# Kernel tuning notes

Measured on AMD Instinct MI355X. Metric: run time of the kernel, lower is better.

The kernel has to match this reference:

```python
import jax, jax.numpy as jnp
import numpy as np

B, M, K, F, H = 4096, 50000, 31, 256, 256
N = K + 1                      # nodes per graph: center + K neighbors
GAMMA = 1.0 / (2.0 * 1.0 ** 2) # rbf_kernel gamma with length_scale = 1.0


def setup_inputs() -> dict:
    key = jax.random.key(0)
    k = jax.random.split(key, 9)
    return {
        "spatial_features": jax.random.normal(k[0], (B, 2), jnp.float32),
        "features": jax.random.normal(k[1], (B, F), jnp.float32),
        "train_spatial": jax.random.normal(k[2], (M, 2), jnp.float32),
        "train_features": jax.random.normal(k[3], (M, F), jnp.float32),
        "train_y": jax.random.normal(k[4], (M, 1), jnp.float32),
        "W0": jax.random.normal(k[5], (F + 2, H), jnp.float32) * (1.0 / np.sqrt(F + 2)),
        "W1": jax.random.normal(k[6], (H, H), jnp.float32) * (1.0 / np.sqrt(H)),
        "W2": jax.random.normal(k[7], (H, H), jnp.float32) * (1.0 / np.sqrt(H)),
        "Wout": jax.random.normal(k[8], (H, 1), jnp.float32) * (1.0 / np.sqrt(H)),
    }


def reference(spatial_features, features, train_spatial, train_features, train_y,
              W0, W1, W2, Wout):
    # --- brute-force kNN over train spatial coords (sklearn kneighbors) ---
    d2 = (jnp.sum(spatial_features ** 2, -1, keepdims=True)
          - 2.0 * spatial_features @ train_spatial.T
          + jnp.sum(train_spatial ** 2, -1)[None, :])                 # [B, M]
    nb = jax.lax.top_k(jax.lax.stop_gradient(-d2), K)[1]              # [B, K] indices

    # --- form_input_graph: node features = [feat ++ y ++ indicator] ---
    feat = jnp.concatenate([features[:, None, :], train_features[nb]], axis=1)    # [B,N,F]
    y = jnp.concatenate([jnp.zeros((B, 1, 1), feat.dtype), train_y[nb]], axis=1)  # [B,N,1]
    ind = jnp.zeros((B, N, 1), feat.dtype).at[:, 0, 0].set(1.0)                   # [B,N,1]
    x = jnp.concatenate([feat, y, ind], axis=-1)                                  # [B,N,F+2]

    # --- dense RBF adjacency: complete graph, self-loops already on diagonal ---
    coords = jnp.concatenate([spatial_features[:, None, :], train_spatial[nb]], axis=1)  # [B,N,2]
    diff = coords[:, :, None, :] - coords[:, None, :, :]
    A = jnp.exp(-GAMMA * jnp.sum(diff * diff, -1))                    # [B,N,N]
    # GCN symmetric normalization D^-1/2 A D^-1/2 (deg > 0 since diag = 1)
    dinv = jax.lax.rsqrt(jnp.sum(A, -1))                              # [B,N]
    Ahat = A * dinv[:, :, None] * dinv[:, None, :]

    h = jax.nn.relu(jnp.einsum('bij,bjh->bih', Ahat, x @ W0))
    h = jax.nn.relu(jnp.einsum('bij,bjh->bih', Ahat, h @ W1))
    h = jax.nn.relu(jnp.einsum('bij,bjh->bih', Ahat, h @ W2))

    # center node -> linear head (bias=False), last_activation='none'
    return h[:, 0] @ Wout                                             # [B, 1]
```

## Files before the change

### kernel.cpp

```cpp
#include <hip/hip_runtime.h>

typedef _Float16 half8 __attribute__((ext_vector_type(8)));
typedef __fp16  fp16x2 __attribute__((ext_vector_type(2)));
typedef float f32x16 __attribute__((ext_vector_type(16)));

#define M_TRAIN 50000
#define NQ 4096
#define KNN 31

#define LO_SCALE 1024.0f
#define LO_INV   9.765625e-4f

__global__ void prep_weights_k(const float* __restrict__ W0,
                               const float* __restrict__ W1,
                               const float* __restrict__ W2,
                               _Float16* __restrict__ W0hi, _Float16* __restrict__ W0lo,
                               _Float16* __restrict__ W1hi, _Float16* __restrict__ W1lo,
                               _Float16* __restrict__ W2hi, _Float16* __restrict__ W2lo) {
    int t = blockIdx.x * 256 + threadIdx.x;
    const int n0 = 17 * 8 * 64, n1 = 16 * 8 * 64, n2 = 16 * 8 * 64;
    if (t >= n0 + n1 + n2) return;
    const float* src; _Float16 *dhi, *dlo; int idx, Kin;
    if (t < n0)           { src = W0; dhi = W0hi; dlo = W0lo; idx = t;           Kin = 258; }
    else if (t < n0 + n1) { src = W1; dhi = W1hi; dlo = W1lo; idx = t - n0;      Kin = 256; }
    else                  { src = W2; dhi = W2hi; dlo = W2lo; idx = t - n0 - n1; Kin = 256; }
    int lane = idx & 63, nt = (idx >> 6) & 7, ks = idx >> 9;
    int col = nt * 32 + (lane & 31);
    int k0  = ks * 16 + (lane >> 5) * 8;
    _Float16 vhi[8], vlo[8];
#pragma unroll
    for (int j = 0; j < 8; j++) {
        int k = k0 + j;
        float w = (k < Kin) ? src[k * 256 + col] : 0.f;
        _Float16 hi = (_Float16)w;
        vhi[j] = hi;
        vlo[j] = (_Float16)((w - (float)hi) * LO_SCALE);
    }
    *reinterpret_cast<uint4*>(dhi + (size_t)idx * 8) = *reinterpret_cast<const uint4*>(vhi);
    *reinterpret_cast<uint4*>(dlo + (size_t)idx * 8) = *reinterpret_cast<const uint4*>(vlo);
}

#define QPB2 4
#define TILE2 2048
#define CAP2 128

__global__ __launch_bounds__(256) void knn_k(const float* __restrict__ qs,
                                             const float* __restrict__ ts,
                                             int* __restrict__ nb) {
    __shared__ __align__(16) float tile[TILE2 * 2];
    __shared__ float  mrg[QPB2][128];
    __shared__ int    ci[QPB2][CAP2];
    __shared__ double chd[QPB2][CAP2];
    __shared__ int    cnt[QPB2];

    const int t = threadIdx.x;
    const int w = t >> 6, lane = t & 63;
    const int q = blockIdx.x * QPB2 + w;

    if (lane == 0) cnt[w] = 0;
    const float qx = qs[q * 2 + 0], qy = qs[q * 2 + 1];
    const float2* tilev = reinterpret_cast<const float2*>(tile);

    float v0 = 3.4e38f, v1 = 3.4e38f;
    for (int base = 0; base < M_TRAIN; base += TILE2) {
        const int n = min(TILE2, M_TRAIN - base);
        __syncthreads();
        for (int i = t; i < n / 2; i += 256)
            reinterpret_cast<float4*>(tile)[i] =
                reinterpret_cast<const float4*>(ts + (size_t)base * 2)[i];
        __syncthreads();
#pragma unroll 4
        for (int p = lane; p < n; p += 64) {
            float2 pt = tilev[p];
            float dx = qx - pt.x, dy = qy - pt.y;
            float d2 = fmaf(dx, dx, dy * dy);
            v1 = fminf(v1, fmaxf(v0, d2));
            v0 = fminf(v0, d2);
        }
    }
    __syncthreads();
    mrg[w][2 * lane]     = v0;
    mrg[w][2 * lane + 1] = v1;
    __syncthreads();

    float xa = mrg[w][lane], xb = mrg[w][64 + lane];
    int lea = 0, leb = 0;
    for (int i = 0; i < 128; i++) {
        float v = mrg[w][i];
        lea += (v <= xa) ? 1 : 0;
        leb += (v <= xb) ? 1 : 0;
    }
    float tc = 3.4e38f;
    if (lea >= 31) tc = xa;
    if (leb >= 31 && xb < tc) tc = xb;
#pragma unroll
    for (int off = 32; off; off >>= 1)
        tc = fminf(tc, __shfl_xor(tc, off));
    const float thr = tc * 1.00001f + 1e-7f;

    for (int base = 0; base < M_TRAIN; base += TILE2) {
        const int n = min(TILE2, M_TRAIN - base);
        __syncthreads();
        for (int i = t; i < n / 2; i += 256)
            reinterpret_cast<float4*>(tile)[i] =
                reinterpret_cast<const float4*>(ts + (size_t)base * 2)[i];
        __syncthreads();
#pragma unroll 4
        for (int p = lane; p < n; p += 64) {
            float2 pt = tilev[p];
            float dx = qx - pt.x, dy = qy - pt.y;
            float d2 = fmaf(dx, dx, dy * dy);
            if (d2 < thr) {
                int pos = atomicAdd(&cnt[w], 1);
                if (pos < CAP2) ci[w][pos] = base + p;
            }
        }
    }
    __syncthreads();

    const int C = min(cnt[w], CAP2);
    for (int c = lane; c < C; c += 64) {
        int idx = ci[w][c];
        double dx = (double)qx - (double)ts[idx * 2];
        double dy = (double)qy - (double)ts[idx * 2 + 1];
        chd[w][c] = dx * dx + dy * dy;
    }
    __syncthreads();
    for (int c = lane; c < C; c += 64) {
        double key = chd[w][c];
        int   idx = ci[w][c];
        int rank = 0;
        for (int o = 0; o < C; o++) {
            double ok = chd[w][o];
            int    oi = ci[w][o];
            rank += ((ok < key) || (ok == key && oi < idx)) ? 1 : 0;
        }
        if (rank < KNN) nb[q * KNN + rank] = idx;
    }
}

#define PX 276
#define PT 36

__device__ inline half8 ld_h8(const _Float16* p) {
    union { half8 h; uint2 u[2]; } r;
    r.u[0] = *reinterpret_cast<const uint2*>(p);
    r.u[1] = *reinterpret_cast<const uint2*>(p + 4);
    return r.h;
}
__device__ inline half8 ld_h8_g(const _Float16* p) {
    union { half8 h; uint4 u; } r;
    r.u = *reinterpret_cast<const uint4*>(p);
    return r.h;
}
__device__ inline f32x16 zero16() {
    f32x16 z;
#pragma unroll
    for (int i = 0; i < 16; i++) z[i] = 0.f;
    return z;
}
__device__ inline unsigned pk_u(float a, float b) {
    union { fp16x2 v; unsigned u; } c;
    c.v = __builtin_amdgcn_cvt_pkrtz(a, b);
    return c.u;
}
__device__ inline float f16lo(unsigned u) {
    union { unsigned u; fp16x2 v; } c; c.u = u; return (float)c.v[0];
}
__device__ inline float f16hi(unsigned u) {
    union { unsigned u; fp16x2 v; } c; c.u = u; return (float)c.v[1];
}
__device__ inline half8 frag_x(const unsigned* w, int ks2, int h) {
    unsigned w0 = w[4 * ks2 + 0], w1 = w[4 * ks2 + 1];
    unsigned w2 = w[4 * ks2 + 2], w3 = w[4 * ks2 + 3];
    unsigned sA = h ? w0 : w2, sB = h ? w1 : w3;
    unsigned rA = __shfl_xor(sA, 32);
    unsigned rB = __shfl_xor(sB, 32);
    unsigned kA = h ? w2 : w0, kB = h ? w3 : w1;
    union { half8 h8; unsigned u[4]; } f;
    f.u[0] = h ? rA : kA;
    f.u[1] = h ? rB : kB;
    f.u[2] = h ? kA : rA;
    f.u[3] = h ? kB : rB;
    return f.h8;
}
#define MFMA(a, b, c) __builtin_amdgcn_mfma_f32_32x32x16_f16((a), (b), (c), 0, 0, 0)

__global__ __launch_bounds__(512, 4) void gcn_k(
    const float* __restrict__ qs, const float* __restrict__ qf,
    const float* __restrict__ ts, const float* __restrict__ tf,
    const float* __restrict__ ty, const float* __restrict__ Wout,
    const int* __restrict__ nb,
    const _Float16* __restrict__ W0hi, const _Float16* __restrict__ W0lo,
    const _Float16* __restrict__ W1hi, const _Float16* __restrict__ W1lo,
    const _Float16* __restrict__ W2hi, const _Float16* __restrict__ W2lo,
    float* __restrict__ out) {
    __shared__ __align__(16) _Float16 Xhi[64 * PX];
    __shared__ __align__(16) _Float16 Xlo[64 * PX];
    __shared__ _Float16 Ahhi[2 * 32 * PT];
    __shared__ _Float16 Ahlo[2 * 32 * PT];
    __shared__ float coords[128];
    __shared__ float dinv[64];
    __shared__ float yvs[64];
    __shared__ int   idxs[64];

    const int t = threadIdx.x;
    const int w = t >> 6, lane = t & 63;
    const int h = lane >> 5, ln = lane & 31;
    const int g2 = blockIdx.x * 2;

    if (t < 64) {
        int g = t >> 5, n = t & 31;
        int idx = (n == 0) ? -1 : nb[(g2 + g) * KNN + (n - 1)];
        idxs[t] = idx;
        const float* c = (n == 0) ? (qs + (size_t)(g2 + g) * 2) : (ts + (size_t)idx * 2);
        coords[t * 2 + 0] = c[0];
        coords[t * 2 + 1] = c[1];
        yvs[t] = (n == 0) ? 0.f : ty[idx];
    }
    __syncthreads();

    {
        const float* s0 = ((w & 31) == 0) ? (qf + (size_t)(g2 + (w >> 5)) * 256)
                                          : (tf + (size_t)idxs[w] * 256);
        float4 pv = reinterpret_cast<const float4*>(s0)[lane];
        for (int r = w; r < 64; r += 8) {
            float4 cv = pv;
            int rn = r + 8;
            if (rn < 64) {
                const float* sn = ((rn & 31) == 0) ? (qf + (size_t)(g2 + (rn >> 5)) * 256)
                                                   : (tf + (size_t)idxs[rn] * 256);
                pv = reinterpret_cast<const float4*>(sn)[lane];
            }
            float a4[4] = {cv.x, cv.y, cv.z, cv.w};
            unsigned hw[2], lw[2];
#pragma unroll
            for (int j = 0; j < 2; j++) {
                float x0 = a4[2 * j], x1 = a4[2 * j + 1];
                hw[j] = pk_u(x0, x1);
                lw[j] = pk_u((x0 - f16lo(hw[j])) * LO_SCALE,
                             (x1 - f16hi(hw[j])) * LO_SCALE);
            }
            *reinterpret_cast<uint2*>(&Xhi[r * PX + 4 * lane]) = *reinterpret_cast<uint2*>(hw);
            *reinterpret_cast<uint2*>(&Xlo[r * PX + 4 * lane]) = *reinterpret_cast<uint2*>(lw);
            if (lane == 0) {
                float yv = yvs[r];
                _Float16 thi[16], tlo[16];
#pragma unroll
                for (int j = 0; j < 16; j++) { thi[j] = (_Float16)0.f; tlo[j] = (_Float16)0.f; }
                _Float16 yh = (_Float16)yv;
                thi[0] = yh;
                tlo[0] = (_Float16)((yv - (float)yh) * LO_SCALE);
                thi[1] = ((r & 31) == 0) ? (_Float16)1.f : (_Float16)0.f;
#pragma unroll
                for (int c = 0; c < 4; c++) {
                    *reinterpret_cast<uint2*>(&Xhi[r * PX + 256 + 4 * c]) = reinterpret_cast<uint2*>(thi)[c];
                    *reinterpret_cast<uint2*>(&Xlo[r * PX + 256 + 4 * c]) = reinterpret_cast<uint2*>(tlo)[c];
                }
            }
        }
    }

    if (t < 128) {
        int g = t >> 6, i = (t >> 1) & 31, jh = t & 1;
        int ni = g * 32 + i;
        float xi = coords[ni * 2], yi = coords[ni * 2 + 1];
        float part = 0.f;
#pragma unroll
        for (int jj = 0; jj < 16; jj++) {
            int nj = g * 32 + jh * 16 + jj;
            float dx = xi - coords[nj * 2], dy = yi - coords[nj * 2 + 1];
            part += __expf(-0.5f * (dx * dx + dy * dy));
        }
        float asum = part + __shfl_xor(part, 1);
        if (jh == 0) dinv[ni] = 1.0f / sqrtf(asum);
    }
    __syncthreads();
    if (t < 128) {
        int g = t >> 6, i = (t >> 1) & 31, jh = t & 1;
        int ni = g * 32 + i;
        float xi = coords[ni * 2], yi = coords[ni * 2 + 1];
        float di = dinv[ni];
        _Float16 ahi[16], alo[16];
#pragma unroll
        for (int jj = 0; jj < 16; jj++) {
            int nj = g * 32 + jh * 16 + jj;
            float dx = xi - coords[nj * 2], dy = yi - coords[nj * 2 + 1];
            float a = __expf(-0.5f * (dx * dx + dy * dy)) * di * dinv[nj];
            _Float16 hi = (_Float16)a;
            ahi[jj] = hi;
            alo[jj] = (_Float16)((a - (float)hi) * LO_SCALE);
        }
        _Float16* dh = &Ahhi[ni * PT + jh * 16];
        _Float16* dl = &Ahlo[ni * PT + jh * 16];
#pragma unroll
        for (int c = 0; c < 4; c++) {
            reinterpret_cast<uint2*>(dh)[c] = reinterpret_cast<uint2*>(ahi)[c];
            reinterpret_cast<uint2*>(dl)[c] = reinterpret_cast<uint2*>(alo)[c];
        }
    }
    __syncthreads();

    const _Float16* Whis[3] = {W0hi, W1hi, W2hi};
    const _Float16* Wlos[3] = {W0lo, W1lo, W2lo};
    for (int layer = 0; layer < 3; layer++) {
        const _Float16* Whi = Whis[layer];
        const _Float16* Wlo = Wlos[layer];
        const int KS = (layer == 0) ? 17 : 16;

        f32x16 acc0 = zero16(), cor0 = zero16();
        f32x16 acc1 = zero16(), cor1 = zero16();
        const int boBase = (w * 64 + lane) * 8;
        const _Float16* Xa0 = &Xhi[ln * PX + 8 * h];
        const _Float16* Xb0 = &Xlo[ln * PX + 8 * h];
        const _Float16* Xa1 = &Xhi[(32 + ln) * PX + 8 * h];
        const _Float16* Xb1 = &Xlo[(32 + ln) * PX + 8 * h];
#pragma unroll 2
        for (int ks = 0; ks < KS; ks++) {
            int bo = boBase + ks * 4096;
            half8 Bh = ld_h8_g(Whi + bo);
            half8 Bl = ld_h8_g(Wlo + bo);
            half8 A0h = ld_h8(Xa0 + ks * 16);
            half8 A0l = ld_h8(Xb0 + ks * 16);
            half8 A1h = ld_h8(Xa1 + ks * 16);
            half8 A1l = ld_h8(Xb1 + ks * 16);
            acc0 = MFMA(A0h, Bh, acc0);
            cor0 = MFMA(A0l, Bh, cor0);
            cor0 = MFMA(A0h, Bl, cor0);
            acc1 = MFMA(A1h, Bh, acc1);
            cor1 = MFMA(A1l, Bh, cor1);
            cor1 = MFMA(A1h, Bl, cor1);
        }
        __syncthreads();

        unsigned whi0[8], wlo0[8], whi1[8], wlo1[8];
#pragma unroll
        for (int g = 0; g < 8; g++) {
            float x0 = fmaf(cor0[2 * g],     LO_INV, acc0[2 * g]);
            float x1 = fmaf(cor0[2 * g + 1], LO_INV, acc0[2 * g + 1]);
            unsigned hw = pk_u(x0, x1);
            whi0[g] = hw;
            wlo0[g] = pk_u((x0 - f16lo(hw)) * LO_SCALE, (x1 - f16hi(hw)) * LO_SCALE);
            float y0 = fmaf(cor1[2 * g],     LO_INV, acc1[2 * g]);
            float y1 = fmaf(cor1[2 * g + 1], LO_INV, acc1[2 * g + 1]);
            unsigned hv = pk_u(y0, y1);
            whi1[g] = hv;
            wlo1[g] = pk_u((y0 - f16lo(hv)) * LO_SCALE, (y1 - f16hi(hv)) * LO_SCALE);
        }

        f32x16 p0 = zero16(), pc0 = zero16();
        f32x16 p1 = zero16(), pc1 = zero16();
#pragma unroll
        for (int ks2 = 0; ks2 < 2; ks2++) {
            half8 bA0h = ld_h8(&Ahhi[ln * PT + ks2 * 16 + 8 * h]);
            half8 bA0l = ld_h8(&Ahlo[ln * PT + ks2 * 16 + 8 * h]);
            half8 bA1h = ld_h8(&Ahhi[(32 + ln) * PT + ks2 * 16 + 8 * h]);
            half8 bA1l = ld_h8(&Ahlo[(32 + ln) * PT + ks2 * 16 + 8 * h]);
            half8 t0hi = frag_x(whi0, ks2, h);
            half8 t0lo = frag_x(wlo0, ks2, h);
            half8 t1hi = frag_x(whi1, ks2, h);
            half8 t1lo = frag_x(wlo1, ks2, h);
            p0  = MFMA(t0hi, bA0h, p0);
            pc0 = MFMA(t0lo, bA0h, pc0);
            pc0 = MFMA(t0hi, bA0l, pc0);
            p1  = MFMA(t1hi, bA1h, p1);
            pc1 = MFMA(t1lo, bA1h, pc1);
            pc1 = MFMA(t1hi, bA1l, pc1);
        }

#pragma unroll
        for (int g = 0; g < 2; g++) {
            const f32x16& P = g ? p1 : p0;
            const f32x16& C = g ? pc1 : pc0;
            int row = g * 32 + ln;
#pragma unroll
            for (int c = 0; c < 4; c++) {
                float x0 = fmaf(C[4 * c + 0], LO_INV, P[4 * c + 0]);
                float x1 = fmaf(C[4 * c + 1], LO_INV, P[4 * c + 1]);
                float x2 = fmaf(C[4 * c + 2], LO_INV, P[4 * c + 2]);
                float x3 = fmaf(C[4 * c + 3], LO_INV, P[4 * c + 3]);
                x0 = fmaxf(x0, 0.f); x1 = fmaxf(x1, 0.f);
                x2 = fmaxf(x2, 0.f); x3 = fmaxf(x3, 0.f);
                unsigned hw[2], lw[2];
                hw[0] = pk_u(x0, x1);
                hw[1] = pk_u(x2, x3);
                lw[0] = pk_u((x0 - f16lo(hw[0])) * LO_SCALE, (x1 - f16hi(hw[0])) * LO_SCALE);
                lw[1] = pk_u((x2 - f16lo(hw[1])) * LO_SCALE, (x3 - f16hi(hw[1])) * LO_SCALE);
                int feat = 32 * w + 8 * c + 4 * h;
                *reinterpret_cast<uint2*>(&Xhi[row * PX + feat]) = *reinterpret_cast<uint2*>(hw);
                *reinterpret_cast<uint2*>(&Xlo[row * PX + feat]) = *reinterpret_cast<uint2*>(lw);
            }
        }
        __syncthreads();
    }

    if (w < 2) {
        float4 wv = reinterpret_cast<const float4*>(Wout)[lane];
        union { uint2 u; _Float16 f[4]; } hh, hl;
        hh.u = *reinterpret_cast<const uint2*>(&Xhi[(w * 32) * PX + 4 * lane]);
        hl.u = *reinterpret_cast<const uint2*>(&Xlo[(w * 32) * PX + 4 * lane]);
        float s = ((float)hh.f[0] + (float)hl.f[0] * LO_INV) * wv.x
                + ((float)hh.f[1] + (float)hl.f[1] * LO_INV) * wv.y
                + ((float)hh.f[2] + (float)hl.f[2] * LO_INV) * wv.z
                + ((float)hh.f[3] + (float)hl.f[3] * LO_INV) * wv.w;
#pragma unroll
        for (int off = 32; off; off >>= 1) s += __shfl_xor(s, off);
        if (lane == 0) out[g2 + w] = s;
    }
}

extern "C" void kernel_launch(void* const* d_in, const int* in_sizes, int n_in,
                              void* d_out, int out_size, void* d_ws, size_t ws_size,
                              hipStream_t stream) {
    const float* qs   = (const float*)d_in[0];
    const float* qf   = (const float*)d_in[1];
    const float* ts   = (const float*)d_in[2];
    const float* tf   = (const float*)d_in[3];
    const float* ty   = (const float*)d_in[4];
    const float* W0   = (const float*)d_in[5];
    const float* W1   = (const float*)d_in[6];
    const float* W2   = (const float*)d_in[7];
    const float* Wout = (const float*)d_in[8];
    float* out = (float*)d_out;

    char* ws = (char*)d_ws;
    int*      nb   = (int*)ws;
    _Float16* W0hi = (_Float16*)(ws + 524288);
    _Float16* W0lo = (_Float16*)(ws + 663552);
    _Float16* W1hi = (_Float16*)(ws + 802816);
    _Float16* W1lo = (_Float16*)(ws + 933888);
    _Float16* W2hi = (_Float16*)(ws + 1064960);
    _Float16* W2lo = (_Float16*)(ws + 1196032);

    hipLaunchKernelGGL(prep_weights_k, dim3(98), dim3(256), 0, stream,
                       W0, W1, W2, W0hi, W0lo, W1hi, W1lo, W2hi, W2lo);
    hipLaunchKernelGGL(knn_k, dim3(NQ / QPB2), dim3(256), 0, stream, qs, ts, nb);
    hipLaunchKernelGGL(gcn_k, dim3(NQ / 2), dim3(512), 0, stream,
                       qs, qf, ts, tf, ty, Wout, nb,
                       W0hi, W0lo, W1hi, W1lo, W2hi, W2lo, out);
}
```

Baseline: 315.9 us.

## Process two queries per wave in kNN and widen MFMA loop unroll

Each wave in the kNN kernel now handles two queries and reads two train points per float4 LDS load, so each loaded tile element serves twice the distance work and the block count halves. The per-lane candidate summary drops from a 2-smallest pair to a single minimum over 64 lanes for threshold selection, which may loosen the threshold and admit more candidates against the fixed cap. Separately, the GCN layer K-loop unroll goes from 2 to 4 to expose more MFMA/load overlap, at some register cost.

Measured after the change: 328.2 us. +3.9%, slower.

```diff
diff --git a/kernel.cpp b/kernel.cpp
--- a/kernel.cpp
+++ b/kernel.cpp
@@ -40,7 +40,7 @@
     *reinterpret_cast<uint4*>(dlo + (size_t)idx * 8) = *reinterpret_cast<const uint4*>(vlo);
 }
 
-#define QPB2 4
+#define QPB2 8
 #define TILE2 2048
 #define CAP2 128
 
@@ -48,20 +48,20 @@
                                              const float* __restrict__ ts,
                                              int* __restrict__ nb) {
     __shared__ __align__(16) float tile[TILE2 * 2];
-    __shared__ float  mrg[QPB2][128];
+    __shared__ float  mrg[QPB2][64];
     __shared__ int    ci[QPB2][CAP2];
     __shared__ double chd[QPB2][CAP2];
     __shared__ int    cnt[QPB2];
 
     const int t = threadIdx.x;
     const int w = t >> 6, lane = t & 63;
-    const int q = blockIdx.x * QPB2 + w;
-
-    if (lane == 0) cnt[w] = 0;
-    const float qx = qs[q * 2 + 0], qy = qs[q * 2 + 1];
-    const float2* tilev = reinterpret_cast<const float2*>(tile);
-
-    float v0 = 3.4e38f, v1 = 3.4e38f;
+    const int qA = blockIdx.x * QPB2 + 2 * w, qB = qA + 1;
+
+    if (lane < 2) cnt[2 * w + lane] = 0;
+    const float qxA = qs[qA * 2 + 0], qyA = qs[qA * 2 + 1];
+    const float qxB = qs[qB * 2 + 0], qyB = qs[qB * 2 + 1];
+
+    float vA = 3.4e38f, vB = 3.4e38f;
     for (int base = 0; base < M_TRAIN; base += TILE2) {
         const int n = min(TILE2, M_TRAIN - base);
         __syncthreads();
@@ -70,33 +70,42 @@
                 reinterpret_cast<const float4*>(ts + (size_t)base * 2)[i];
         __syncthreads();
 #pragma unroll 4
-        for (int p = lane; p < n; p += 64) {
-            float2 pt = tilev[p];
-            float dx = qx - pt.x, dy = qy - pt.y;
-            float d2 = fmaf(dx, dx, dy * dy);
-            v1 = fminf(v1, fmaxf(v0, d2));
-            v0 = fminf(v0, d2);
-        }
-    }
-    __syncthreads();
-    mrg[w][2 * lane]     = v0;
-    mrg[w][2 * lane + 1] = v1;
-    __syncthreads();
-
-    float xa = mrg[w][lane], xb = mrg[w][64 + lane];
-    int lea = 0, leb = 0;
-    for (int i = 0; i < 128; i++) {
-        float v = mrg[w][i];
-        lea += (v <= xa) ? 1 : 0;
-        leb += (v <= xb) ? 1 : 0;
-    }
-    float tc = 3.4e38f;
-    if (lea >= 31) tc = xa;
-    if (leb >= 31 && xb < tc) tc = xb;
-#pragma unroll
-    for (int off = 32; off; off >>= 1)
-        tc = fminf(tc, __shfl_xor(tc, off));
-    const float thr = tc * 1.00001f + 1e-7f;
+        for (int p = 2 * lane; p < n; p += 128) {
+            float4 pt = *reinterpret_cast<const float4*>(&tile[2 * p]);
+            float dxA0 = qxA - pt.x, dyA0 = qyA - pt.y;
+            float dxA1 = qxA - pt.z, dyA1 = qyA - pt.w;
+            float dA0 = fmaf(dxA0, dxA0, dyA0 * dyA0);
+            float dA1 = fmaf(dxA1, dxA1, dyA1 * dyA1);
+            vA = fminf(vA, fminf(dA0, dA1));
+            float dxB0 = qxB - pt.x, dyB0 = qyB - pt.y;
+            float dxB1 = qxB - pt.z, dyB1 = qyB - pt.w;
+            float dB0 = fmaf(dxB0, dxB0, dyB0 * dyB0);
+            float dB1 = fmaf(dxB1, dxB1, dyB1 * dyB1);
+            vB = fminf(vB, fminf(dB0, dB1));
+        }
+    }
+    __syncthreads();
+    mrg[2 * w + 0][lane] = vA;
+    mrg[2 * w + 1][lane] = vB;
+    __syncthreads();
+
+    float thrq[2];
+#pragma unroll
+    for (int qq = 0; qq < 2; qq++) {
+        const int qi = 2 * w + qq;
+        float x = mrg[qi][lane];
+        int le = 0;
+        for (int i = 0; i < 64; i++) {
+            float v = mrg[qi][i];
+            le += (v <= x) ? 1 : 0;
+        }
+        float tc = (le >= 31) ? x : 3.4e38f;
+#pragma unroll
+        for (int off = 32; off; off >>= 1)
+            tc = fminf(tc, __shfl_xor(tc, off));
+        thrq[qq] = tc * 1.00001f + 1e-7f;
+    }
+    const float thrA = thrq[0], thrB = thrq[1];
 
     for (int base = 0; base < M_TRAIN; base += TILE2) {
         const int n = min(TILE2, M_TRAIN - base);
@@ -106,36 +115,61 @@
                 reinterpret_cast<const float4*>(ts + (size_t)base * 2)[i];
         __syncthreads();
 #pragma unroll 4
-        for (int p = lane; p < n; p += 64) {
-            float2 pt = tilev[p];
-            float dx = qx - pt.x, dy = qy - pt.y;
-            float d2 = fmaf(dx, dx, dy * dy);
-            if (d2 < thr) {
-                int pos = atomicAdd(&cnt[w], 1);
-                if (pos < CAP2) ci[w][pos] = base + p;
-            }
-        }
-    }
-    __syncthreads();
-
-    const int C = min(cnt[w], CAP2);
-    for (int c = lane; c < C; c += 64) {
-        int idx = ci[w][c];
-        double dx = (double)qx - (double)ts[idx * 2];
-        double dy = (double)qy - (double)ts[idx * 2 + 1];
-        chd[w][c] = dx * dx + dy * dy;
-    }
-    __syncthreads();
-    for (int c = lane; c < C; c += 64) {
-        double key = chd[w][c];
-        int   idx = ci[w][c];
-        int rank = 0;
-        for (int o = 0; o < C; o++) {
-            double ok = chd[w][o];
-            int    oi = ci[w][o];
-            rank += ((ok < key) || (ok == key && oi < idx)) ? 1 : 0;
-        }
-        if (rank < KNN) nb[q * KNN + rank] = idx;
+        for (int p = 2 * lane; p < n; p += 128) {
+            float4 pt = *reinterpret_cast<const float4*>(&tile[2 * p]);
+            float dxA0 = qxA - pt.x, dyA0 = qyA - pt.y;
+            float dxA1 = qxA - pt.z, dyA1 = qyA - pt.w;
+            float dA0 = fmaf(dxA0, dxA0, dyA0 * dyA0);
+            float dA1 = fmaf(dxA1, dxA1, dyA1 * dyA1);
+            if (dA0 < thrA) {
+                int pos = atomicAdd(&cnt[2 * w + 0], 1);
+                if (pos < CAP2) ci[2 * w + 0][pos] = base + p;
+            }
+            if (dA1 < thrA) {
+                int pos = atomicAdd(&cnt[2 * w + 0], 1);
+                if (pos < CAP2) ci[2 * w + 0][pos] = base + p + 1;
+            }
+            float dxB0 = qxB - pt.x, dyB0 = qyB - pt.y;
+            float dxB1 = qxB - pt.z, dyB1 = qyB - pt.w;
+            float dB0 = fmaf(dxB0, dxB0, dyB0 * dyB0);
+            float dB1 = fmaf(dxB1, dxB1, dyB1 * dyB1);
+            if (dB0 < thrB) {
+                int pos = atomicAdd(&cnt[2 * w + 1], 1);
+                if (pos < CAP2) ci[2 * w + 1][pos] = base + p;
+            }
+            if (dB1 < thrB) {
+                int pos = atomicAdd(&cnt[2 * w + 1], 1);
+                if (pos < CAP2) ci[2 * w + 1][pos] = base + p + 1;
+            }
+        }
+    }
+    __syncthreads();
+
+#pragma unroll
+    for (int qq = 0; qq < 2; qq++) {
+        const int qi = 2 * w + qq;
+        const int q  = qA + qq;
+        const float qx = qq ? qxB : qxA, qy = qq ? qyB : qyA;
+        const int C = min(cnt[qi], CAP2);
+        for (int c = lane; c < C; c += 64) {
+            int idx = ci[qi][c];
+            double dx = (double)qx - (double)ts[idx * 2];
+            double dy = (double)qy - (double)ts[idx * 2 + 1];
+            chd[qi][c] = dx * dx + dy * dy;
+        }
+        __syncthreads();
+        for (int c = lane; c < C; c += 64) {
+            double key = chd[qi][c];
+            int   idx = ci[qi][c];
+            int rank = 0;
+            for (int o = 0; o < C; o++) {
+                double ok = chd[qi][o];
+                int    oi = ci[qi][o];
+                rank += ((ok < key) || (ok == key && oi < idx)) ? 1 : 0;
+            }
+            if (rank < KNN) nb[q * KNN + rank] = idx;
+        }
+        __syncthreads();
     }
 }
 
@@ -315,7 +349,7 @@
         const _Float16* Xb0 = &Xlo[ln * PX + 8 * h];
         const _Float16* Xa1 = &Xhi[(32 + ln) * PX + 8 * h];
         const _Float16* Xb1 = &Xlo[(32 + ln) * PX + 8 * h];
-#pragma unroll 2
+#pragma unroll 4
         for (int ks = 0; ks < KS; ks++) {
             int bo = boBase + ks * 4096;
             half8 Bh = ld_h8_g(Whi + bo);
```

## Halve GCN block to 4 waves, each computing a 64-column register tile

Applied to the files above, without the earlier changes.

The GCN kernel now launches 256-thread blocks instead of 512. Each wave computes two 32-column output tiles instead of one, so the X fragments read from LDS are reused across twice as many MFMAs. The feature-load loop strides by 4 waves instead of 8. The aim is to cut LDS fragment traffic and per-block scheduling overhead. In exchange, accumulator register usage roughly doubles and there are fewer waves per block to hide latency.

Result: slower. 334.8 us (+6.0%).

```diff
diff --git a/kernel.cpp b/kernel.cpp
--- a/kernel.cpp
+++ b/kernel.cpp
@@ -186,7 +186,7 @@
 }
 #define MFMA(a, b, c) __builtin_amdgcn_mfma_f32_32x32x16_f16((a), (b), (c), 0, 0, 0)
 
-__global__ __launch_bounds__(512, 4) void gcn_k(
+__global__ __launch_bounds__(256, 2) void gcn_k(
     const float* __restrict__ qs, const float* __restrict__ qf,
     const float* __restrict__ ts, const float* __restrict__ tf,
     const float* __restrict__ ty, const float* __restrict__ Wout,
@@ -221,12 +221,13 @@
     __syncthreads();
 
     {
-        const float* s0 = ((w & 31) == 0) ? (qf + (size_t)(g2 + (w >> 5)) * 256)
+        const float* s0 = ((w & 31) == 0) ? (qf + (size_t)(g2 + 0) * 2 * 128)
                                           : (tf + (size_t)idxs[w] * 256);
+        if (w == 0) s0 = qf + (size_t)g2 * 256;
         float4 pv = reinterpret_cast<const float4*>(s0)[lane];
-        for (int r = w; r < 64; r += 8) {
+        for (int r = w; r < 64; r += 4) {
             float4 cv = pv;
-            int rn = r + 8;
+            int rn = r + 4;
             if (rn < 64) {
                 const float* sn = ((rn & 31) == 0) ? (qf + (size_t)(g2 + (rn >> 5)) * 256)
                                                    : (tf + (size_t)idxs[rn] * 256);
@@ -308,9 +309,13 @@
         const _Float16* Wlo = Wlos[layer];
         const int KS = (layer == 0) ? 17 : 16;
 
-        f32x16 acc0 = zero16(), cor0 = zero16();
-        f32x16 acc1 = zero16(), cor1 = zero16();
-        const int boBase = (w * 64 + lane) * 8;
+        f32x16 acc[2][2], cor[2][2];
+#pragma unroll
+        for (int g = 0; g < 2; g++)
+#pragma unroll
+            for (int n = 0; n < 2; n++) { acc[g][n] = zero16(); cor[g][n] = zero16(); }
+
+        const int boBase = (2 * w * 64 + lane) * 8;
         const _Float16* Xa0 = &Xhi[ln * PX + 8 * h];
         const _Float16* Xb0 = &Xlo[ln * PX + 8 * h];
         const _Float16* Xa1 = &Xhi[(32 + ln) * PX + 8 * h];
@@ -318,79 +323,93 @@
 #pragma unroll 2
         for (int ks = 0; ks < KS; ks++) {
             int bo = boBase + ks * 4096;
-            half8 Bh = ld_h8_g(Whi + bo);
-            half8 Bl = ld_h8_g(Wlo + bo);
+            half8 Bh0 = ld_h8_g(Whi + bo);
+            half8 Bh1 = ld_h8_g(Whi + bo + 512);
+            half8 Bl0 = ld_h8_g(Wlo + bo);
+            half8 Bl1 = ld_h8_g(Wlo + bo + 512);
             half8 A0h = ld_h8(Xa0 + ks * 16);
             half8 A0l = ld_h8(Xb0 + ks * 16);
             half8 A1h = ld_h8(Xa1 + ks * 16);
             half8 A1l = ld_h8(Xb1 + ks * 16);
-            acc0 = MFMA(A0h, Bh, acc0);
-            cor0 = MFMA(A0l, Bh, cor0);
-            cor0 = MFMA(A0h, Bl, cor0);
-            acc1 = MFMA(A1h, Bh, acc1);
-            cor1 = MFMA(A1l, Bh, cor1);
-            cor1 = MFMA(A1h, Bl, cor1);
-        }
-        __syncthreads();
-
-        unsigned whi0[8], wlo0[8], whi1[8], wlo1[8];
-#pragma unroll
-        for (int g = 0; g < 8; g++) {
-            float x0 = fmaf(cor0[2 * g],     LO_INV, acc0[2 * g]);
-            float x1 = fmaf(cor0[2 * g + 1], LO_INV, acc0[2 * g + 1]);
-            unsigned hw = pk_u(x0, x1);
-            whi0[g] = hw;
-            wlo0[g] = pk_u((x0 - f16lo(hw)) * LO_SCALE, (x1 - f16hi(hw)) * LO_SCALE);
-            float y0 = fmaf(cor1[2 * g],     LO_INV, acc1[2 * g]);
-            float y1 = fmaf(cor1[2 * g + 1], LO_INV, acc1[2 * g + 1]);
-            unsigned hv = pk_u(y0, y1);
-            whi1[g] = hv;
-            wlo1[g] = pk_u((y0 - f16lo(hv)) * LO_SCALE, (y1 - f16hi(hv)) * LO_SCALE);
-        }
-
-        f32x16 p0 = zero16(), pc0 = zero16();
-        f32x16 p1 = zero16(), pc1 = zero16();
+            acc[0][0] = MFMA(A0h, Bh0, acc[0][0]);
+            cor[0][0] = MFMA(A0l, Bh0, cor[0][0]);
+            cor[0][0] = MFMA(A0h, Bl0, cor[0][0]);
+            acc[0][1] = MFMA(A0h, Bh1, acc[0][1]);
+            cor[0][1] = MFMA(A0l, Bh1, cor[0][1]);
+            cor[0][1] = MFMA(A0h, Bl1, cor[0][1]);
+            acc[1][0] = MFMA(A1h, Bh0, acc[1][0]);
+            cor[1][0] = MFMA(A1l, Bh0, cor[1][0]);
+            cor[1][0] = MFMA(A1h, Bl0, cor[1][0]);
+            acc[1][1] = MFMA(A1h, Bh1, acc[1][1]);
+            cor[1][1] = MFMA(A1l, Bh1, cor[1][1]);
+            cor[1][1] = MFMA(A1h, Bl1, cor[1][1]);
+        }
+        __syncthreads();
+
+        unsigned whi[2][2][8], wlo[2][2][8];
+#pragma unroll
+        for (int g = 0; g < 2; g++)
+#pragma unroll
+            for (int n = 0; n < 2; n++)
+#pragma unroll
+                for (int gg = 0; gg < 8; gg++) {
+                    float x0 = fmaf(cor[g][n][2 * gg],     LO_INV, acc[g][n][2 * gg]);
+                    float x1 = fmaf(cor[g][n][2 * gg + 1], LO_INV, acc[g][n][2 * gg + 1]);
+                    unsigned hw = pk_u(x0, x1);
+                    whi[g][n][gg] = hw;
+                    wlo[g][n][gg] = pk_u((x0 - f16lo(hw)) * LO_SCALE,
+                                         (x1 - f16hi(hw)) * LO_SCALE);
+                }
+
+        f32x16 p[2][2], pc[2][2];
+#pragma unroll
+        for (int g = 0; g < 2; g++)
+#pragma unroll
+            for (int n = 0; n < 2; n++) { p[g][n] = zero16(); pc[g][n] = zero16(); }
 #pragma unroll
         for (int ks2 = 0; ks2 < 2; ks2++) {
             half8 bA0h = ld_h8(&Ahhi[ln * PT + ks2 * 16 + 8 * h]);
             half8 bA0l = ld_h8(&Ahlo[ln * PT + ks2 * 16 + 8 * h]);
             half8 bA1h = ld_h8(&Ahhi[(32 + ln) * PT + ks2 * 16 + 8 * h]);
             half8 bA1l = ld_h8(&Ahlo[(32 + ln) * PT + ks2 * 16 + 8 * h]);
-            half8 t0hi = frag_x(whi0, ks2, h);
-            half8 t0lo = frag_x(wlo0, ks2, h);
-            half8 t1hi = frag_x(whi1, ks2, h);
-            half8 t1lo = frag_x(wlo1, ks2, h);
-            p0  = MFMA(t0hi, bA0h, p0);
-            pc0 = MFMA(t0lo, bA0h, pc0);
-            pc0 = MFMA(t0hi, bA0l, pc0);
-            p1  = MFMA(t1hi, bA1h, p1);
-            pc1 = MFMA(t1lo, bA1h, pc1);
-            pc1 = MFMA(t1hi, bA1l, pc1);
-        }
-
-#pragma unroll
-        for (int g = 0; g < 2; g++) {
-            const f32x16& P = g ? p1 : p0;
-            const f32x16& C = g ? pc1 : pc0;
-            int row = g * 32 + ln;
-#pragma unroll
-            for (int c = 0; c < 4; c++) {
-                float x0 = fmaf(C[4 * c + 0], LO_INV, P[4 * c + 0]);
-                float x1 = fmaf(C[4 * c + 1], LO_INV, P[4 * c + 1]);
-                float x2 = fmaf(C[4 * c + 2], LO_INV, P[4 * c + 2]);
-                float x3 = fmaf(C[4 * c + 3], LO_INV, P[4 * c + 3]);
-                x0 = fmaxf(x0, 0.f); x1 = fmaxf(x1, 0.f);
-                x2 = fmaxf(x2, 0.f); x3 = fmaxf(x3, 0.f);
-                unsigned hw[2], lw[2];
-                hw[0] = pk_u(x0, x1);
-                hw[1] = pk_u(x2, x3);
-                lw[0] = pk_u((x0 - f16lo(hw[0])) * LO_SCALE, (x1 - f16hi(hw[0])) * LO_SCALE);
-                lw[1] = pk_u((x2 - f16lo(hw[1])) * LO_SCALE, (x3 - f16hi(hw[1])) * LO_SCALE);
-                int feat = 32 * w + 8 * c + 4 * h;
-                *reinterpret_cast<uint2*>(&Xhi[row * PX + feat]) = *reinterpret_cast<uint2*>(hw);
-                *reinterpret_cast<uint2*>(&Xlo[row * PX + feat]) = *reinterpret_cast<uint2*>(lw);
-            }
-        }
+#pragma unroll
+            for (int n = 0; n < 2; n++) {
+                half8 t0hi = frag_x(whi[0][n], ks2, h);
+                half8 t0lo = frag_x(wlo[0][n], ks2, h);
+                half8 t1hi = frag_x(whi[1][n], ks2, h);
+                half8 t1lo = frag_x(wlo[1][n], ks2, h);
+                p[0][n]  = MFMA(t0hi, bA0h, p[0][n]);
+                pc[0][n] = MFMA(t0lo, bA0h, pc[0][n]);
+                pc[0][n] = MFMA(t0hi, bA0l, pc[0][n]);
+                p[1][n]  = MFMA(t1hi, bA1h, p[1][n]);
+                pc[1][n] = MFMA(t1lo, bA1h, pc[1][n]);
+                pc[1][n] = MFMA(t1hi, bA1l, pc[1][n]);
+            }
+        }
+
+#pragma unroll
+        for (int g = 0; g < 2; g++)
+#pragma unroll
+            for (int n = 0; n < 2; n++) {
+                int row = g * 32 + ln;
+#pragma unroll
+                for (int c = 0; c < 4; c++) {
+                    float x0 = fmaf(pc[g][n][4 * c + 0], LO_INV, p[g][n][4 * c + 0]);
+                    float x1 = fmaf(pc[g][n][4 * c + 1], LO_INV, p[g][n][4 * c + 1]);
+                    float x2 = fmaf(pc[g][n][4 * c + 2], LO_INV, p[g][n][4 * c + 2]);
+                    float x3 = fmaf(pc[g][n][4 * c + 3], LO_INV, p[g][n][4 * c + 3]);
+                    x0 = fmaxf(x0, 0.f); x1 = fmaxf(x1, 0.f);
+                    x2 = fmaxf(x2, 0.f); x3 = fmaxf(x3, 0.f);
+                    unsigned hw[2], lw[2];
+                    hw[0] = pk_u(x0, x1);
+                    hw[1] = pk_u(x2, x3);
+                    lw[0] = pk_u((x0 - f16lo(hw[0])) * LO_SCALE, (x1 - f16hi(hw[0])) * LO_SCALE);
+                    lw[1] = pk_u((x2 - f16lo(hw[1])) * LO_SCALE, (x3 - f16hi(hw[1])) * LO_SCALE);
+                    int feat = 64 * w + 32 * n + 8 * c + 4 * h;
+                    *reinterpret_cast<uint2*>(&Xhi[row * PX + feat]) = *reinterpret_cast<uint2*>(hw);
+                    *reinterpret_cast<uint2*>(&Xlo[row * PX + feat]) = *reinterpret_cast<uint2*>(lw);
+                }
+            }
         __syncthreads();
     }
 
@@ -435,7 +454,7 @@
     hipLaunchKernelGGL(prep_weights_k, dim3(98), dim3(256), 0, stream,
                        W0, W1, W2, W0hi, W0lo, W1hi, W1lo, W2hi, W2lo);
     hipLaunchKernelGGL(knn_k, dim3(NQ / QPB2), dim3(256), 0, stream, qs, ts, nb);
-    hipLaunchKernelGGL(gcn_k, dim3(NQ / 2), dim3(512), 0, stream,
+    hipLaunchKernelGGL(gcn_k, dim3(NQ / 2), dim3(256), 0, stream,
                        qs, qf, ts, tf, ty, Wout, nb,
                        W0hi, W0lo, W1hi, W1lo, W2hi, W2lo, out);
 }
```
